# Optimization experiments

Hardware: AMD Instinct MI355X
Metric: run time of the kernel (lower is better)

## Reference

```python
import jax, jax.numpy as jnp
import numpy as np

B, S, D, H = 4, 2048, 1024, 16
HD = D // H
EPS = 1e-7  # K.epsilon()


def setup_inputs() -> dict:
    key = jax.random.key(0)
    ks = jax.random.split(key, 5)
    scale = 1.0 / np.sqrt(D)  # keep projections numerically tame (glorot-ish)
    return {
        "x": jax.random.normal(ks[0], (B, S, D), dtype=jnp.float32),
        "Wq": jax.random.normal(ks[1], (D, D), dtype=jnp.float32) * scale,
        "bq": jnp.zeros((D,), dtype=jnp.float32),
        "Wk": jax.random.normal(ks[2], (D, D), dtype=jnp.float32) * scale,
        "bk": jnp.zeros((D,), dtype=jnp.float32),
        "Wv": jax.random.normal(ks[3], (D, D), dtype=jnp.float32) * scale,
        "bv": jnp.zeros((D,), dtype=jnp.float32),
        "Wo": jax.random.normal(ks[4], (D, D), dtype=jnp.float32) * scale,
        "bo": jnp.zeros((D,), dtype=jnp.float32),
    }


def _split_heads(t):
    # [B,S,D] -> [B,H,S,HD]
    return t.reshape(B, S, H, HD).transpose(0, 2, 1, 3)


def reference(x, Wq, bq, Wk, bk, Wv, bv, Wo, bo):
    relu = jax.nn.relu
    # projections with post-activation (keras layer applies activation to each mapping)
    q = _split_heads(relu(x @ Wq + bq))
    k = _split_heads(relu(x @ Wk + bk))
    v = _split_heads(relu(x @ Wv + bv))
    # scaled dot-product scores, scale = sqrt(head_dim)
    e = jnp.einsum("bhqd,bhkd->bhqk", q, k) / jnp.sqrt(jnp.asarray(HD, x.dtype))
    # exp with row max over ALL keys (before masking), as in the source
    e = jnp.exp(e - jnp.max(e, axis=-1, keepdims=True))
    # history_only: multiplicative causal mask applied AFTER exp
    causal = (jnp.arange(S)[None, :] <= jnp.arange(S)[:, None]).astype(x.dtype)
    e = e * causal  # broadcasts over [B,H,S,S]
    a = e / (jnp.sum(e, axis=-1, keepdims=True) + EPS)
    ctx = jnp.einsum("bhqk,bhkd->bhqd", a, v)
    y = ctx.transpose(0, 2, 1, 3).reshape(B, S, D)  # merge heads
    return relu(y @ Wo + bo)
```

## Files before the change

### kernel.cpp

```cpp
#include <hip/hip_runtime.h>
#include <hip/hip_bf16.h>
#include <cstdint>
#include <cstddef>

#define B_  4
#define S_  2048
#define D_  1024
#define H_  16
#define HD_ 64

typedef _Float16 half8  __attribute__((ext_vector_type(8)));
typedef _Float16 half4v __attribute__((ext_vector_type(4)));
typedef float    f32x4  __attribute__((ext_vector_type(4)));

__device__ __forceinline__ void async_copy16(const void* g, void* l) {
    __builtin_amdgcn_global_load_lds(
        (const __attribute__((address_space(1))) unsigned int*)g,
        (__attribute__((address_space(3))) unsigned int*)l,
        16, 0, 0);
}

__device__ __forceinline__ half8 hscale8(half8 v, _Float16 s) {
    #pragma unroll
    for (int i = 0; i < 8; ++i) v[i] *= s;
    return v;
}


__global__ void cast_x_kernel(const float4* __restrict__ in, half4v* __restrict__ out, int n4) {
    int i = blockIdx.x * 256 + threadIdx.x;
    if (i < n4) {
        float4 v = in[i];
        half4v h = { (_Float16)v.x, (_Float16)v.y, (_Float16)v.z, (_Float16)v.w };
        out[i] = h;
    }
}

__global__ void transpose_cast4_kernel(
    const float* __restrict__ W0, const float* __restrict__ W1,
    const float* __restrict__ W2, const float* __restrict__ W3,
    _Float16* __restrict__ T0, _Float16* __restrict__ T1,
    _Float16* __restrict__ T2, _Float16* __restrict__ T3)
{
    __shared__ float tile[32][33];
    const float* Wsel[4] = { W0, W1, W2, W3 };
    _Float16*    Tsel[4] = { T0, T1, T2, T3 };
    const float* W  = Wsel[blockIdx.z];
    _Float16*    Wt = Tsel[blockIdx.z];
    const int bn = blockIdx.x * 32, bk = blockIdx.y * 32;
    const int tx = threadIdx.x, ty = threadIdx.y;
    #pragma unroll
    for (int i = 0; i < 32; i += 8)
        tile[ty + i][tx] = W[(size_t)(bk + ty + i) * D_ + bn + tx];
    __syncthreads();
    #pragma unroll
    for (int i = 0; i < 32; i += 8)
        Wt[(size_t)(bn + ty + i) * D_ + bk + tx] = (_Float16)tile[tx][ty + i];
}

template<int OUT_MODE>
__global__ __launch_bounds__(256, 2) void gemm_bt_kernel(
    const _Float16* __restrict__ A, const _Float16* __restrict__ Bt,
    const float* __restrict__ b0, const float* __restrict__ b1,
    const float* __restrict__ b2,
    void* __restrict__ C0, void* __restrict__ C1, void* __restrict__ C2,
    int M, int N, int K)
{
    __shared__ _Float16 As[128 * 64];
    __shared__ _Float16 Bs[128 * 64];
    const int tid  = threadIdx.x;
    const int wid  = tid >> 6, lane = tid & 63;
    const int lr   = lane & 15, lq = lane >> 4;
    const int m0   = blockIdx.x * 128, n0 = blockIdx.y * 128;
    const int wm   = (wid >> 1) * 64, wn = (wid & 1) * 64;
    const int srow = tid >> 3;
    const int csw  = ((tid & 7) ^ (srow & 7)) * 8;

    f32x4 acc[4][4] = {};

    for (int k0 = 0; k0 < K; k0 += 64) {
        __syncthreads();
        #pragma unroll
        for (int i = 0; i < 4; ++i) {
            async_copy16(A  + (size_t)(m0 + i * 32 + srow) * K + k0 + csw,
                         (char*)As + (i * 256 + wid * 64) * 16);
            async_copy16(Bt + (size_t)(n0 + i * 32 + srow) * K + k0 + csw,
                         (char*)Bs + (i * 256 + wid * 64) * 16);
        }
        __syncthreads();
        #pragma unroll
        for (int ks = 0; ks < 2; ++ks) {
            half8 af[4], bf[4];
            #pragma unroll
            for (int t = 0; t < 4; ++t) {
                af[t] = *(const half8*)(As + (wm + t * 16 + lr) * 64 + (((ks * 4 + lq) ^ (lr & 7)) * 8));
                bf[t] = *(const half8*)(Bs + (wn + t * 16 + lr) * 64 + (((ks * 4 + lq) ^ (lr & 7)) * 8));
            }
            #pragma unroll
            for (int mt = 0; mt < 4; ++mt)
                #pragma unroll
                for (int nt = 0; nt < 4; ++nt)
                    acc[mt][nt] = __builtin_amdgcn_mfma_f32_16x16x32_f16(
                        af[mt], bf[nt], acc[mt][nt], 0, 0, 0);
        }
    }

    const int seg = (OUT_MODE == 3) ? (n0 >> 10) : 0;
    const float* bp = (OUT_MODE == 3) ? (seg == 0 ? b0 : (seg == 1 ? b1 : b2)) : b0;

    #pragma unroll
    for (int mt = 0; mt < 4; ++mt) {
        const int row = m0 + wm + mt * 16 + lq * 4;
        #pragma unroll
        for (int nt = 0; nt < 4; ++nt) {
            const int col = n0 + wn + nt * 16 + lr;
            const int cl  = (OUT_MODE == 3) ? (col & 1023) : col;
            const float bb = bp[cl];
            if (OUT_MODE == 3 && seg == 2) {
                const int b = row >> 11, sq = row & 2047;
                const int h = cl >> 6, hd = cl & 63;
                half4v o;
                #pragma unroll
                for (int r = 0; r < 4; ++r) {
                    float v = acc[mt][nt][r] + bb;
                    o[r] = (_Float16)(v > 0.0f ? v : 0.0f);
                }
                *(half4v*)((_Float16*)C2 +
                           ((size_t)(b * 16 + h) * 64 + hd) * S_ + sq) = o;
            } else if (OUT_MODE == 3) {
                _Float16* dst = (_Float16*)(seg ? C1 : C0);
                #pragma unroll
                for (int r = 0; r < 4; ++r) {
                    float v = acc[mt][nt][r] + bb;
                    dst[(size_t)(row + r) * 1024 + cl] = (_Float16)(v > 0.0f ? v : 0.0f);
                }
            } else {
                #pragma unroll
                for (int r = 0; r < 4; ++r) {
                    float v = acc[mt][nt][r] + bb;
                    ((float*)C0)[(size_t)(row + r) * N + col] = v > 0.0f ? v : 0.0f;
                }
            }
        }
    }
}

__global__ __launch_bounds__(256, 2) void attn_kernel(
    const _Float16* __restrict__ Qg, const _Float16* __restrict__ Kg,
    const _Float16* __restrict__ Vtg, _Float16* __restrict__ Y)
{
    __shared__ _Float16 Ks[2][64 * 64];
    __shared__ _Float16 Vt[2][64 * 64];
    __shared__ _Float16 Ps[4][4][16 * 64];

    const int i  = blockIdx.x;
    const int bh = ((i & 7) << 3) | (i >> 6);
    const int p  = (i >> 3) & 7;
    const int b  = bh >> 4, h = bh & 15;
    const int tid = threadIdx.x, wid = tid >> 6, lane = tid & 63;
    const int lr = lane & 15, lq = lane >> 4;

    const size_t base  = ((size_t)b * S_) * D_ + (size_t)h * HD_;
    const _Float16* Vh = Vtg + (size_t)bh * 64 * S_;

    const int srow = tid >> 3;
    const int csw  = ((tid & 7) ^ (srow & 7)) * 8;

    const int L = 128 * p, Hh = 1920 - 128 * p;
    const int qb[4] = { L + 16 * wid, L + 64 + 16 * wid,
                        Hh + 16 * wid, Hh + 64 + 16 * wid };
    const int dk[4] = { 2 * p, 2 * p + 1, 30 - 2 * p, 31 - 2 * p };
    const int nIter = 32 - 2 * p;

    half8 aq[4][2];
    #pragma unroll
    for (int f = 0; f < 4; ++f) {
        const _Float16* qp = Qg + base + (size_t)(qb[f] + lr) * D_;
        aq[f][0] = hscale8(*(const half8*)(qp + lq * 8),      (_Float16)0.18033688f);
        aq[f][1] = hscale8(*(const half8*)(qp + 32 + lq * 8), (_Float16)0.18033688f);
    }

    float lsum[4] = {};
    f32x4 O[4][4] = {};

    auto issue_tile = [&](int kb) {
        const int bufi = kb & 1;
        #pragma unroll
        for (int ii = 0; ii < 2; ++ii) {
            async_copy16(Kg + base + (size_t)(kb * 64 + ii * 32 + srow) * D_ + csw,
                         (char*)Ks[bufi] + (ii * 256 + wid * 64) * 16);
            async_copy16(Vh + (size_t)(ii * 32 + srow) * S_ + kb * 64 + csw,
                         (char*)Vt[bufi] + (ii * 256 + wid * 64) * 16);
        }
    };

    issue_tile(0);

    for (int kb = 0; kb < nIter; ++kb) {
        const int cur = kb & 1;
        __syncthreads();
        if (kb + 1 < nIter) issue_tile(kb + 1);

        const _Float16* Kc = Ks[cur];
        const _Float16* Vc = Vt[cur];

        half8 kf[2][4];
        #pragma unroll
        for (int ks = 0; ks < 2; ++ks)
            #pragma unroll
            for (int t = 0; t < 4; ++t)
                kf[ks][t] = *(const half8*)(Kc + (t * 16 + lr) * 64 + (((ks * 4 + lq) ^ (lr & 7)) * 8));

        #pragma unroll
        for (int f = 0; f < 4; ++f) {
            if (kb > dk[f]) continue;

            f32x4 sc[4] = {};
            #pragma unroll
            for (int ks = 0; ks < 2; ++ks)
                #pragma unroll
                for (int t = 0; t < 4; ++t)
                    sc[t] = __builtin_amdgcn_mfma_f32_16x16x32_f16(kf[ks][t], aq[f][ks], sc[t], 0, 0, 0);

            const bool diag = (kb == dk[f]);
            const int qg = qb[f] + lr;
            const int kbase = kb * 64 + lq * 4;
            float sum = 0.0f;
            _Float16* pw = Ps[wid][f];
            #pragma unroll
            for (int t = 0; t < 4; ++t) {
                half4v pv;
                #pragma unroll
                for (int r = 0; r < 4; ++r) {
                    float ev = __builtin_amdgcn_exp2f(fminf(sc[t][r] - 5.770780f, 15.8696f));
                    if (diag)
                        ev = (kbase + t * 16 + r <= qg) ? ev : 0.0f;
                    pv[r] = (_Float16)ev;
                    sum += ev;
                }
                *(half4v*)(pw + lr * 64 + (((t * 2 + (lq >> 1)) ^ (lr & 7)) * 8) + (lq & 1) * 4) = pv;
            }
            lsum[f] += sum;
        }

        asm volatile("s_waitcnt lgkmcnt(0)" ::: "memory");

        half8 bv[2][4];
        #pragma unroll
        for (int ks = 0; ks < 2; ++ks)
            #pragma unroll
            for (int t = 0; t < 4; ++t)
                bv[ks][t] = *(const half8*)(Vc + (t * 16 + lr) * 64 + (((ks * 4 + lq) ^ (lr & 7)) * 8));

        #pragma unroll
        for (int f = 0; f < 4; ++f) {
            if (kb > dk[f]) continue;
            const _Float16* pw = Ps[wid][f];
            #pragma unroll
            for (int ks = 0; ks < 2; ++ks) {
                half8 ap = *(const half8*)(pw + lr * 64 + (((ks * 4 + lq) ^ (lr & 7)) * 8));
                #pragma unroll
                for (int t = 0; t < 4; ++t)
                    O[f][t] = __builtin_amdgcn_mfma_f32_16x16x32_f16(ap, bv[ks][t], O[f][t], 0, 0, 0);
            }
        }
    }

    #pragma unroll
    for (int f = 0; f < 4; ++f) {
        float tot = lsum[f];
        tot += __shfl_xor(tot, 16);
        tot += __shfl_xor(tot, 32);
        const int q0 = qb[f] + lq * 4;
        #pragma unroll
        for (int r = 0; r < 4; ++r) {
            const float inv = 1.0f / (__shfl(tot, lq * 4 + r) + 1e-7f);
            #pragma unroll
            for (int nt = 0; nt < 4; ++nt)
                Y[base + (size_t)(q0 + r) * D_ + nt * 16 + lr] = (_Float16)(O[f][nt][r] * inv);
        }
    }
}


extern "C" void kernel_launch(void* const* d_in, const int* in_sizes, int n_in,
                              void* d_out, int out_size, void* d_ws, size_t ws_size,
                              hipStream_t stream) {
    const float* x  = (const float*)d_in[0];
    const float* Wq = (const float*)d_in[1];
    const float* bq = (const float*)d_in[2];
    const float* Wk = (const float*)d_in[3];
    const float* bk = (const float*)d_in[4];
    const float* Wv = (const float*)d_in[5];
    const float* bv = (const float*)d_in[6];
    const float* Wo = (const float*)d_in[7];
    const float* bo = (const float*)d_in[8];

    char* ws = (char*)d_ws;
    _Float16* xh  = (_Float16*)ws;
    _Float16* wtq = (_Float16*)(ws + (size_t)16777216);
    _Float16* wtk = wtq + 1048576;
    _Float16* wtv = wtk + 1048576;
    _Float16* wto = wtv + 1048576;
    _Float16* Qh  = (_Float16*)(ws + (size_t)16777216 + 4 * (size_t)2097152);
    _Float16* Kh  = Qh + 8388608;
    _Float16* Vth = Kh + 8388608;
    _Float16* Yh  = Vth + 8388608;
    float* out = (float*)d_out;

    cast_x_kernel<<<8192, 256, 0, stream>>>((const float4*)x, (half4v*)xh, 2097152);
    transpose_cast4_kernel<<<dim3(32, 32, 4), dim3(32, 8), 0, stream>>>(
        Wq, Wk, Wv, Wo, wtq, wtk, wtv, wto);

    gemm_bt_kernel<3><<<dim3(64, 24), 256, 0, stream>>>(
        xh, wtq, bq, bk, bv, Qh, Kh, Vth, 8192, 3072, 1024);

    attn_kernel<<<512, 256, 0, stream>>>(Qh, Kh, Vth, Yh);

    gemm_bt_kernel<0><<<dim3(64, 8), 256, 0, stream>>>(
        Yh, wto, bo, bo, bo, out, out, out, 8192, 1024, 1024);
}
```

Before: 258.3 us.

## Keep P in registers via permlane swaps and halve per-block query work

The attention kernel no longer stages the softmax probabilities through shared memory. The exp results are packed to fp16 and rearranged into MFMA A-operand layout with permlane32/permlane16 swaps. Each block now handles two 64-row query tiles (one low, one high, for causal balance) instead of four, the grid doubles to 1024 blocks, and launch bounds rise to 4 blocks per SM. This removes the LDS round trip and its wait, and raises occupancy. The cost is that each K/V tile loaded into shared memory is reused across fewer query rows.

New measurement: 279.3 us. +8.1%, slower.

```diff
diff --git a/kernel.cpp b/kernel.cpp
--- a/kernel.cpp
+++ b/kernel.cpp
@@ -11,7 +11,10 @@
 
 typedef _Float16 half8  __attribute__((ext_vector_type(8)));
 typedef _Float16 half4v __attribute__((ext_vector_type(4)));
+typedef _Float16 half2v __attribute__((ext_vector_type(2)));
 typedef float    f32x4  __attribute__((ext_vector_type(4)));
+typedef unsigned int uint2v __attribute__((ext_vector_type(2)));
+typedef unsigned int uint4v __attribute__((ext_vector_type(4)));
 
 __device__ __forceinline__ void async_copy16(const void* g, void* l) {
     __builtin_amdgcn_global_load_lds(
@@ -24,6 +27,11 @@
     #pragma unroll
     for (int i = 0; i < 8; ++i) v[i] *= s;
     return v;
+}
+
+__device__ __forceinline__ unsigned int pack2(float a, float b) {
+    half2v h = { (_Float16)a, (_Float16)b };
+    return __builtin_bit_cast(unsigned int, h);
 }
 
 
@@ -145,17 +153,16 @@
     }
 }
 
-__global__ __launch_bounds__(256, 2) void attn_kernel(
+__global__ __launch_bounds__(256, 4) void attn_kernel(
     const _Float16* __restrict__ Qg, const _Float16* __restrict__ Kg,
     const _Float16* __restrict__ Vtg, _Float16* __restrict__ Y)
 {
     __shared__ _Float16 Ks[2][64 * 64];
     __shared__ _Float16 Vt[2][64 * 64];
-    __shared__ _Float16 Ps[4][4][16 * 64];
 
     const int i  = blockIdx.x;
-    const int bh = ((i & 7) << 3) | (i >> 6);
-    const int p  = (i >> 3) & 7;
+    const int bh = ((i & 7) << 3) | (i >> 7);
+    const int tp = (i >> 3) & 15;
     const int b  = bh >> 4, h = bh & 15;
     const int tid = threadIdx.x, wid = tid >> 6, lane = tid & 63;
     const int lr = lane & 15, lq = lane >> 4;
@@ -166,22 +173,21 @@
     const int srow = tid >> 3;
     const int csw  = ((tid & 7) ^ (srow & 7)) * 8;
 
-    const int L = 128 * p, Hh = 1920 - 128 * p;
-    const int qb[4] = { L + 16 * wid, L + 64 + 16 * wid,
-                        Hh + 16 * wid, Hh + 64 + 16 * wid };
-    const int dk[4] = { 2 * p, 2 * p + 1, 30 - 2 * p, 31 - 2 * p };
-    const int nIter = 32 - 2 * p;
-
-    half8 aq[4][2];
-    #pragma unroll
-    for (int f = 0; f < 4; ++f) {
+    const int qb[2] = { 64 * tp + 16 * wid, 2048 - 64 * (tp + 1) + 16 * wid };
+    const int dk[2] = { tp, 31 - tp };
+    const int nIter = 32 - tp;
+
+    half8 aq[2][2];
+    #pragma unroll
+    for (int f = 0; f < 2; ++f) {
         const _Float16* qp = Qg + base + (size_t)(qb[f] + lr) * D_;
         aq[f][0] = hscale8(*(const half8*)(qp + lq * 8),      (_Float16)0.18033688f);
         aq[f][1] = hscale8(*(const half8*)(qp + 32 + lq * 8), (_Float16)0.18033688f);
     }
 
-    float lsum[4] = {};
-    f32x4 O[4][4] = {};
+    float lsum[2] = {};
+    f32x4 O[2][4] = {};
+    half8 apf[2][2];
 
     auto issue_tile = [&](int kb) {
         const int bufi = kb & 1;
@@ -208,66 +214,72 @@
         #pragma unroll
         for (int ks = 0; ks < 2; ++ks)
             #pragma unroll
-            for (int t = 0; t < 4; ++t)
-                kf[ks][t] = *(const half8*)(Kc + (t * 16 + lr) * 64 + (((ks * 4 + lq) ^ (lr & 7)) * 8));
-
-        #pragma unroll
-        for (int f = 0; f < 4; ++f) {
+            for (int tt = 0; tt < 4; ++tt)
+                kf[ks][tt] = *(const half8*)(Kc + (tt * 16 + lr) * 64 + (((ks * 4 + lq) ^ (lr & 7)) * 8));
+
+        #pragma unroll
+        for (int f = 0; f < 2; ++f) {
             if (kb > dk[f]) continue;
 
             f32x4 sc[4] = {};
             #pragma unroll
             for (int ks = 0; ks < 2; ++ks)
                 #pragma unroll
-                for (int t = 0; t < 4; ++t)
-                    sc[t] = __builtin_amdgcn_mfma_f32_16x16x32_f16(kf[ks][t], aq[f][ks], sc[t], 0, 0, 0);
+                for (int tt = 0; tt < 4; ++tt)
+                    sc[tt] = __builtin_amdgcn_mfma_f32_16x16x32_f16(kf[ks][tt], aq[f][ks], sc[tt], 0, 0, 0);
 
             const bool diag = (kb == dk[f]);
             const int qg = qb[f] + lr;
             const int kbase = kb * 64 + lq * 4;
             float sum = 0.0f;
-            _Float16* pw = Ps[wid][f];
-            #pragma unroll
-            for (int t = 0; t < 4; ++t) {
-                half4v pv;
+            unsigned int pk[4][2];
+            #pragma unroll
+            for (int tt = 0; tt < 4; ++tt) {
+                float ev[4];
                 #pragma unroll
                 for (int r = 0; r < 4; ++r) {
-                    float ev = __builtin_amdgcn_exp2f(fminf(sc[t][r] - 5.770780f, 15.8696f));
+                    float e = __builtin_amdgcn_exp2f(fminf(sc[tt][r] - 5.770780f, 15.8696f));
                     if (diag)
-                        ev = (kbase + t * 16 + r <= qg) ? ev : 0.0f;
-                    pv[r] = (_Float16)ev;
-                    sum += ev;
+                        e = (kbase + tt * 16 + r <= qg) ? e : 0.0f;
+                    ev[r] = e;
+                    sum += e;
                 }
-                *(half4v*)(pw + lr * 64 + (((t * 2 + (lq >> 1)) ^ (lr & 7)) * 8) + (lq & 1) * 4) = pv;
+                pk[tt][0] = pack2(ev[0], ev[1]);
+                pk[tt][1] = pack2(ev[2], ev[3]);
             }
             lsum[f] += sum;
-        }
-
-        asm volatile("s_waitcnt lgkmcnt(0)" ::: "memory");
+
+            #pragma unroll
+            for (int ks = 0; ks < 2; ++ks) {
+                uint2v s1 = __builtin_amdgcn_permlane32_swap(pk[2 * ks][0], pk[2 * ks + 1][0], false, false);
+                uint2v s2 = __builtin_amdgcn_permlane16_swap(s1[0], s1[1], false, false);
+                uint2v u1 = __builtin_amdgcn_permlane32_swap(pk[2 * ks][1], pk[2 * ks + 1][1], false, false);
+                uint2v u2 = __builtin_amdgcn_permlane16_swap(u1[0], u1[1], false, false);
+                uint4v d = { s2[0], u2[0], s2[1], u2[1] };
+                apf[f][ks] = __builtin_bit_cast(half8, d);
+            }
+        }
 
         half8 bv[2][4];
         #pragma unroll
         for (int ks = 0; ks < 2; ++ks)
             #pragma unroll
-            for (int t = 0; t < 4; ++t)
-                bv[ks][t] = *(const half8*)(Vc + (t * 16 + lr) * 64 + (((ks * 4 + lq) ^ (lr & 7)) * 8));
-
-        #pragma unroll
-        for (int f = 0; f < 4; ++f) {
+            for (int tt = 0; tt < 4; ++tt)
+                bv[ks][tt] = *(const half8*)(Vc + (tt * 16 + lr) * 64 + (((ks * 4 + lq) ^ (lr & 7)) * 8));
+
+        #pragma unroll
+        for (int f = 0; f < 2; ++f) {
             if (kb > dk[f]) continue;
-            const _Float16* pw = Ps[wid][f];
-            #pragma unroll
-            for (int ks = 0; ks < 2; ++ks) {
-                half8 ap = *(const half8*)(pw + lr * 64 + (((ks * 4 + lq) ^ (lr & 7)) * 8));
-                #pragma unroll
-                for (int t = 0; t < 4; ++t)
-                    O[f][t] = __builtin_amdgcn_mfma_f32_16x16x32_f16(ap, bv[ks][t], O[f][t], 0, 0, 0);
-            }
-        }
-    }
-
-    #pragma unroll
-    for (int f = 0; f < 4; ++f) {
+            #pragma unroll
+            for (int ks = 0; ks < 2; ++ks)
+                #pragma unroll
+                for (int tt = 0; tt < 4; ++tt)
+                    O[f][tt] = __builtin_amdgcn_mfma_f32_16x16x32_f16(apf[f][ks], bv[ks][tt], O[f][tt], 0, 0, 0);
+        }
+    }
+
+    #pragma unroll
+    for (int f = 0; f < 2; ++f) {
         float tot = lsum[f];
         tot += __shfl_xor(tot, 16);
         tot += __shfl_xor(tot, 32);
@@ -315,7 +327,7 @@
     gemm_bt_kernel<3><<<dim3(64, 24), 256, 0, stream>>>(
         xh, wtq, bq, bk, bv, Qh, Kh, Vth, 8192, 3072, 1024);
 
-    attn_kernel<<<512, 256, 0, stream>>>(Qh, Kh, Vth, Yh);
+    attn_kernel<<<1024, 256, 0, stream>>>(Qh, Kh, Vth, Yh);
 
     gemm_bt_kernel<0><<<dim3(64, 8), 256, 0, stream>>>(
         Yh, wto, bo, bo, bo, out, out, out, 8192, 1024, 1024);
```
